# Kernel tuning notes

Hardware: AMD Instinct MI355X
Metric: run time of the kernel (lower is better)

## Reference

```python
import jax, jax.numpy as jnp
import numpy as np

B, S, D = 2, 2048, 1024   # batch, seq, hidden_size
H = 512                   # intermediate_size
E, K = 8, 2               # num_local_experts, num_experts_per_tok


def setup_inputs() -> dict:
    key = jax.random.key(0)
    k1, k2, k3, k4 = jax.random.split(key, 4)
    scale = 0.02
    return {
        "layer_input": jax.random.normal(k1, (B, S, D), dtype=jnp.float32),
        "w_router": jax.random.normal(k2, (E, D), dtype=jnp.float32) * scale,   # Linear(D, E, bias=False)
        "w_in": jax.random.normal(k3, (E, 2 * H, D), dtype=jnp.float32) * scale,  # ParallelExperts(E, D, 2H)
        "w_out": jax.random.normal(k4, (E, D, H), dtype=jnp.float32) * scale,     # ParallelExperts(E, H, D)
    }


def reference(layer_input, w_router, w_in, w_out):
    bsz, length, d = layer_input.shape
    x = layer_input.reshape(-1, d)                       # [T, D]
    T = x.shape[0]

    # ---- router (JetMoeTopKGating): top-k logits -> softmax gates ----
    router_logits = x @ w_router.T                       # [T, E], fp32
    top_v, top_i = jax.lax.top_k(router_logits, K)       # [T, K]
    top_gates = jax.nn.softmax(top_v, axis=-1)           # [T, K]
    # sparse gate matrix: zero except selected experts (equivalent to
    # torch's sort/gather/index_add dispatch-combine)
    gates = jnp.zeros((T, E), dtype=x.dtype).at[jnp.arange(T)[:, None], top_i].add(top_gates)  # [T, E]

    # ---- experts: fused SwiGLU FFN per expert; combine with sparse gates ----
    h = jnp.einsum('td,efd->tef', x, w_in)               # [T, E, 2H]
    a, b = jnp.split(h, 2, axis=-1)
    h = jax.nn.silu(a) * b                               # [T, E, H]
    y = jnp.einsum('teh,edh->ted', h, w_out)             # [T, E, D]
    out = jnp.einsum('te,ted->td', gates, y)             # [T, D]

    return out.reshape(bsz, length, d), router_logits
```

## Files before the change

### kernel.cpp

```cpp
#include <hip/hip_runtime.h>

typedef unsigned short u16;
typedef unsigned int   u32;

#define T_TOK 4096
#define D_DIM 1024
#define H_DIM 512
#define E_NUM 8
#define NP1   5120
#define MAXP  5120

typedef __bf16 bf16x8 __attribute__((ext_vector_type(8)));
typedef float  f32x4  __attribute__((ext_vector_type(4)));

__device__ __forceinline__ u16 f2bf(float f) {
    return __builtin_bit_cast(u16, (__bf16)f);
}
__device__ __forceinline__ u32 pk2(float a, float b) {
    return (u32)f2bf(a) | ((u32)f2bf(b) << 16);
}

__device__ __forceinline__ void gll16(const void* g, void* l) {
    __builtin_amdgcn_global_load_lds((const __attribute__((address_space(1))) void*)g,
                                     (__attribute__((address_space(3))) void*)l, 16, 0, 0);
}

#define LDFX(arr, r, ko) __builtin_bit_cast(bf16x8, \
    *(const uint4*)(&arr[r][((((ko) >> 3) ^ ((r) & 7)) << 3)]))
#define MFMA(a, b, c) __builtin_amdgcn_mfma_f32_16x16x32_bf16(a, b, c, 0, 0, 0)

__global__ __launch_bounds__(256) void fused_front(
    const float* __restrict__ x, const float* __restrict__ wr,
    const float* __restrict__ w_in, const float* __restrict__ w_out,
    float* __restrict__ logits_out, int* __restrict__ top_e, float* __restrict__ top_g,
    u16* __restrict__ xb, u16* __restrict__ wib, u16* __restrict__ wob,
    float* __restrict__ out_zero, int* __restrict__ e_init, int* __restrict__ blk_hist)
{
    const int bid = blockIdx.x;
    const int tid = threadIdx.x;

    if (bid >= 256) {
        const int b2 = bid - 256;
        if (b2 < 4096) {
            const size_t i = (size_t)b2 * 256 + tid;
            const float4 a = *(const float4*)(w_in + i * 8);
            const float4 b = *(const float4*)(w_in + i * 8 + 4);
            uint4 o;
            o.x = pk2(a.x, a.y); o.y = pk2(a.z, a.w);
            o.z = pk2(b.x, b.y); o.w = pk2(b.z, b.w);
            *(uint4*)(wib + i * 8) = o;
        } else if (b2 < 6144) {
            const size_t i = (size_t)(b2 - 4096) * 256 + tid;
            const float4 a = *(const float4*)(w_out + i * 8);
            const float4 b = *(const float4*)(w_out + i * 8 + 4);
            uint4 o;
            o.x = pk2(a.x, a.y); o.y = pk2(a.z, a.w);
            o.z = pk2(b.x, b.y); o.w = pk2(b.z, b.w);
            *(uint4*)(wob + i * 8) = o;
        } else if (b2 < 10240) {
            ((float4*)out_zero)[(size_t)(b2 - 6144) * 256 + tid] = make_float4(0.f, 0.f, 0.f, 0.f);
        } else {
            ((int4*)e_init)[(b2 - 10240) * 256 + tid] = make_int4(-1, -1, -1, -1);
        }
        return;
    }

    __shared__ float wrL[E_NUM][1024];
    __shared__ int   bh[16];
    if (tid < 16) bh[tid] = 0;
    #pragma unroll
    for (int i = 0; i < 8; ++i) {
        const int idx = (i * 256 + tid) * 4;
        *(float4*)&wrL[0][idx] = *(const float4*)(wr + idx);
    }
    __syncthreads();

    const int lane = tid & 63;
    const int wv   = tid >> 6;
    const int t0   = bid * 16 + wv * 4;

    for (int tt = 0; tt < 4; ++tt) {
        const int t = t0 + tt;
        const float* xr = x + ((size_t)t << 10);
        float4 xv[4];
        #pragma unroll
        for (int j = 0; j < 4; ++j)
            xv[j] = *(const float4*)(xr + j * 256 + lane * 4);

        #pragma unroll
        for (int j = 0; j < 4; ++j) {
            uint2 p;
            p.x = pk2(xv[j].x, xv[j].y);
            p.y = pk2(xv[j].z, xv[j].w);
            *(uint2*)(xb + ((size_t)t << 10) + j * 256 + lane * 4) = p;
        }

        float acc[E_NUM];
        #pragma unroll
        for (int e = 0; e < E_NUM; ++e) acc[e] = 0.f;
        #pragma unroll
        for (int j = 0; j < 4; ++j) {
            #pragma unroll
            for (int e = 0; e < E_NUM; ++e) {
                const float4 w4 = *(const float4*)&wrL[e][j * 256 + lane * 4];
                acc[e] += xv[j].x * w4.x + xv[j].y * w4.y + xv[j].z * w4.z + xv[j].w * w4.w;
            }
        }
        #pragma unroll
        for (int off = 32; off >= 1; off >>= 1) {
            #pragma unroll
            for (int e = 0; e < E_NUM; ++e)
                acc[e] += __shfl_xor(acc[e], off);
        }
        if (lane == 0) {
            #pragma unroll
            for (int e = 0; e < E_NUM; ++e)
                logits_out[t * E_NUM + e] = acc[e];
            int i0 = 0; float v0 = acc[0];
            #pragma unroll
            for (int e = 1; e < E_NUM; ++e) { if (acc[e] > v0) { v0 = acc[e]; i0 = e; } }
            int i1 = (i0 == 0) ? 1 : 0; float v1 = acc[i1];
            #pragma unroll
            for (int e = 0; e < E_NUM; ++e) { if (e != i0 && e != i1 && acc[e] > v1) { v1 = acc[e]; i1 = e; } }
            const float ed = __expf(v1 - v0);
            const float g0 = 1.f / (1.f + ed);
            top_e[2 * t]     = i0;  top_e[2 * t + 1] = i1;
            top_g[2 * t]     = g0;  top_g[2 * t + 1] = 1.f - g0;
            atomicAdd(&bh[2 * i0],     1);
            atomicAdd(&bh[2 * i1 + 1], 1);
        }
    }
    __syncthreads();
    if (tid < 16) blk_hist[bid * 16 + tid] = bh[tid];
}

__global__ __launch_bounds__(1024) void prep_kernel(
    const int* __restrict__ top_e, int* __restrict__ ws_i,
    int* __restrict__ e0, int* __restrict__ e1, const int* __restrict__ blk_hist)
{
    __shared__ int hist[16];
    __shared__ int cur[16];
    const int tid = threadIdx.x;
    if (tid < 16) hist[tid] = 0;
    __syncthreads();

    int part = 0;
    #pragma unroll
    for (int j = 0; j < 4; ++j) part += blk_hist[j * 1024 + tid];
    part += __shfl_xor(part, 16);
    part += __shfl_xor(part, 32);
    if ((tid & 63) < 16) atomicAdd(&hist[tid & 15], part);
    __syncthreads();

    if (tid == 0) {
        int off_[16];
        int s0 = 0, s1 = 0;
        for (int e = 0; e < E_NUM; ++e) {
            off_[2 * e]     = s0; s0 += (hist[2 * e]     + 127) & ~127;
            off_[2 * e + 1] = s1; s1 += (hist[2 * e + 1] + 127) & ~127;
        }
        int nt1 = 0;
        for (int e = 0; e < E_NUM; ++e) {
            for (int k = 0; k < 2; ++k) {
                const int b  = 2 * e + k;
                const int pc = (hist[b] + 127) & ~127;
                cur[b] = off_[b];
                for (int j = 0; j < pc / 128; ++j) {
                    const int rl = off_[b] + j * 128;
                    if (nt1 < 96) ws_i[512 + nt1++] = (e << 16) | (k * NP1 + rl);
                }
            }
        }
        ws_i[99] = nt1;
    }
    __syncthreads();

    const int4* t4 = (const int4*)top_e;
    const int4 a = t4[2 * tid];
    const int4 b = t4[2 * tid + 1];
    const int v[8] = {a.x, a.y, a.z, a.w, b.x, b.y, b.z, b.w};
    #pragma unroll
    for (int j = 0; j < 8; ++j) {
        const int i  = tid * 8 + j;
        const int bk = 2 * (v[j] & 7) + (j & 1);
        const int pos = atomicAdd(&cur[bk], 1);
        ((j & 1) ? e1 : e0)[pos] = i;
    }
}

__global__ __launch_bounds__(256, 2) void g1_a(
    const u16* __restrict__ xb, const u16* __restrict__ wib,
    const int* __restrict__ ws_i, const int* __restrict__ e0,
    const int* __restrict__ e1, u16* __restrict__ act)
{
    const int nt = ws_i[99];
    if ((int)blockIdx.y >= nt) return;
    const int tile = ws_i[512 + blockIdx.y];
    const int e  = tile >> 16;
    const int rb = tile & 0xFFFF;
    const int nc = blockIdx.x;

    __shared__ __align__(16) u16 xs[128][64];
    __shared__ __align__(16) u16 wt[128][64];
    __shared__ int tokL[128];

    const int tid = threadIdx.x;
    if (tid < 128) {
        const int ent = (rb >= NP1) ? e1[rb - NP1 + tid] : e0[rb + tid];
        tokL[tid] = (ent < 0) ? 0 : (ent >> 1);
    }
    __syncthreads();

    const int wid = tid >> 6, ln = tid & 63, qd = ln >> 4, lm = ln & 15;
    const int wrh = wid >> 1, wch = wid & 1;

    const u16* xsrc[4];
    const u16* wsrc[4];
    const u16* wbase = wib + ((size_t)e << 20);
    #pragma unroll
    for (int j = 0; j < 4; ++j) {
        const int r  = wid * 32 + j * 8 + (ln >> 3);
        const int sg = (ln & 7) ^ (r & 7);
        xsrc[j] = xb + ((size_t)tokL[r] << 10) + (sg << 3);
        const int h = r >> 6, r2 = r & 63;
        const int wrow = (r2 < 32) ? (nc * 64 + h * 32 + r2)
                                   : (512 + nc * 64 + h * 32 + (r2 - 32));
        wsrc[j] = wbase + ((size_t)wrow << 10) + (sg << 3);
    }

    f32x4 acc[4][4];
    #pragma unroll
    for (int i = 0; i < 4; ++i)
        #pragma unroll
        for (int j = 0; j < 4; ++j) acc[i][j] = (f32x4){0.f,0.f,0.f,0.f};

    for (int k0 = 0; k0 < 1024; k0 += 64) {
        #pragma unroll
        for (int j = 0; j < 4; ++j) {
            gll16(xsrc[j] + k0, &xs[wid * 32 + j * 8][0]);
            gll16(wsrc[j] + k0, &wt[wid * 32 + j * 8][0]);
        }
        __syncthreads();
        #pragma unroll
        for (int ki = 0; ki < 2; ++ki) {
            const int ko = ki * 32 + (qd << 3);
            bf16x8 aF[4], bF[4];
            #pragma unroll
            for (int i = 0; i < 4; ++i) aF[i] = LDFX(xs, wrh * 64 + i * 16 + lm, ko);
            #pragma unroll
            for (int j = 0; j < 4; ++j) bF[j] = LDFX(wt, wch * 64 + j * 16 + lm, ko);
            #pragma unroll
            for (int i = 0; i < 4; ++i)
                #pragma unroll
                for (int j = 0; j < 4; ++j)
                    acc[i][j] = MFMA(aF[i], bF[j], acc[i][j]);
        }
        __syncthreads();
    }

    #pragma unroll
    for (int i = 0; i < 4; ++i) {
        #pragma unroll
        for (int j = 0; j < 2; ++j) {
            #pragma unroll
            for (int r = 0; r < 4; ++r) {
                const float a = acc[i][j][r], b = acc[i][j + 2][r];
                const float v = b * a / (1.f + __expf(-a));
                const int row  = wrh * 64 + i * 16 + (qd << 2) + r;
                const int hcol = nc * 64 + wch * 32 + j * 16 + lm;
                act[((size_t)(rb + row) << 9) + hcol] = f2bf(v);
            }
        }
    }
}

__global__ __launch_bounds__(256, 2) void g2_a(
    const u16* __restrict__ act, const u16* __restrict__ wob,
    const int* __restrict__ ws_i, const int* __restrict__ e0,
    const int* __restrict__ e1, const float* __restrict__ top_g,
    float* __restrict__ out)
{
    const int nt = ws_i[99];
    if ((int)blockIdx.y >= nt) return;
    const int tile = ws_i[512 + blockIdx.y];
    const int e  = tile >> 16;
    const int rb = tile & 0xFFFF;
    const int dc = blockIdx.x;

    __shared__ __align__(16) u16 as_[128][64];
    __shared__ __align__(16) u16 wt2[128][64];
    __shared__ int   entL[128];
    __shared__ float gateL[128];

    const int tid = threadIdx.x;
    if (tid < 128) {
        const int ent = (rb >= NP1) ? e1[rb - NP1 + tid] : e0[rb + tid];
        entL[tid]  = ent;
        gateL[tid] = (ent < 0) ? 0.f : top_g[ent];
    }
    __syncthreads();

    const int wid = tid >> 6, ln = tid & 63, qd = ln >> 4, lm = ln & 15;
    const int wrh = wid >> 1, wch = wid & 1;

    const u16* asrc[4];
    const u16* wsrc[4];
    const u16* wbase = wob + ((size_t)e << 19);
    #pragma unroll
    for (int j = 0; j < 4; ++j) {
        const int r  = wid * 32 + j * 8 + (ln >> 3);
        const int sg = (ln & 7) ^ (r & 7);
        asrc[j] = act + ((size_t)(rb + r) << 9) + (sg << 3);
        wsrc[j] = wbase + ((size_t)((dc << 7) + r) << 9) + (sg << 3);
    }

    f32x4 acc[4][4];
    #pragma unroll
    for (int i = 0; i < 4; ++i)
        #pragma unroll
        for (int j = 0; j < 4; ++j) acc[i][j] = (f32x4){0.f,0.f,0.f,0.f};

    for (int k0 = 0; k0 < 512; k0 += 64) {
        #pragma unroll
        for (int j = 0; j < 4; ++j) {
            gll16(asrc[j] + k0, &as_[wid * 32 + j * 8][0]);
            gll16(wsrc[j] + k0, &wt2[wid * 32 + j * 8][0]);
        }
        __syncthreads();
        #pragma unroll
        for (int ki = 0; ki < 2; ++ki) {
            const int ko = ki * 32 + (qd << 3);
            bf16x8 aF[4], bF[4];
            #pragma unroll
            for (int i = 0; i < 4; ++i) aF[i] = LDFX(as_, wrh * 64 + i * 16 + lm, ko);
            #pragma unroll
            for (int j = 0; j < 4; ++j) bF[j] = LDFX(wt2, wch * 64 + j * 16 + lm, ko);
            #pragma unroll
            for (int i = 0; i < 4; ++i)
                #pragma unroll
                for (int j = 0; j < 4; ++j)
                    acc[i][j] = MFMA(aF[i], bF[j], acc[i][j]);
        }
        __syncthreads();
    }

    #pragma unroll
    for (int i = 0; i < 4; ++i) {
        #pragma unroll
        for (int j = 0; j < 4; ++j) {
            #pragma unroll
            for (int r = 0; r < 4; ++r) {
                const int row = wrh * 64 + i * 16 + (qd << 2) + r;
                const int ent = entL[row];
                if (ent >= 0) {
                    const int t   = ent >> 1;
                    const int col = (dc << 7) + wch * 64 + j * 16 + lm;
                    atomicAdd(out + ((size_t)t << 10) + col, gateL[row] * acc[i][j][r]);
                }
            }
        }
    }
}

extern "C" void kernel_launch(void* const* d_in, const int* in_sizes, int n_in,
                              void* d_out, int out_size, void* d_ws, size_t ws_size,
                              hipStream_t stream)
{
    (void)in_sizes; (void)n_in; (void)out_size; (void)ws_size;
    const float* x     = (const float*)d_in[0];
    const float* wr    = (const float*)d_in[1];
    const float* w_in  = (const float*)d_in[2];
    const float* w_out = (const float*)d_in[3];
    float* out = (float*)d_out;

    char* ws = (char*)d_ws;
    int*   ws_i     = (int*)ws;
    int*   e0       = (int*)(ws + 8192);
    int*   e1       = (int*)(ws + 28672);
    int*   top_e    = (int*)(ws + 49152);
    float* top_g    = (float*)(ws + 81920);
    int*   blk_hist = (int*)(ws + 114688);
    u16*   act      = (u16*)(ws + 147456);
    u16*   xb       = (u16*)(ws + 10633216);
    u16*   wib      = (u16*)(ws + 19021824);
    u16*   wob      = (u16*)(ws + 35799040);

    fused_front<<<10506, 256, 0, stream>>>(x, wr, w_in, w_out,
                                           out + (size_t)T_TOK * D_DIM,
                                           top_e, top_g, xb, wib, wob,
                                           out, e0, blk_hist);
    prep_kernel<<<1, 1024, 0, stream>>>(top_e, ws_i, e0, e1, blk_hist);
    g1_a<<<dim3(8, 80), 256, 0, stream>>>(xb, wib, ws_i, e0, e1, act);
    g2_a<<<dim3(8, 80), 256, 0, stream>>>(act, wob, ws_i, e0, e1, top_g, out);
}
```

Before: 183.6 us.

## Replace atomic scatter-add with per-slot bf16 buffer and combine kernel

The second expert GEMM now writes each gated (token, slot) result as bf16 into a scratch buffer indexed by the entry id, instead of doing fp32 atomicAdd into the output. A new combine kernel sums the two slots per token into the output. This also removes the output-zeroing blocks from the front kernel. The aim is to avoid atomic traffic and the zero-fill pass, at the cost of an extra kernel launch, an extra read/write pass, and bf16 rounding of partial results. The y buffer reuses the xb region, which is only safe because xb is dead by then.

```diff
diff --git a/kernel.cpp b/kernel.cpp
--- a/kernel.cpp
+++ b/kernel.cpp
@@ -19,6 +19,9 @@
 __device__ __forceinline__ u32 pk2(float a, float b) {
     return (u32)f2bf(a) | ((u32)f2bf(b) << 16);
 }
+__device__ __forceinline__ float bf2f(u32 lo16) {
+    return __builtin_bit_cast(float, lo16 << 16);
+}
 
 __device__ __forceinline__ void gll16(const void* g, void* l) {
     __builtin_amdgcn_global_load_lds((const __attribute__((address_space(1))) void*)g,
@@ -34,7 +37,7 @@
     const float* __restrict__ w_in, const float* __restrict__ w_out,
     float* __restrict__ logits_out, int* __restrict__ top_e, float* __restrict__ top_g,
     u16* __restrict__ xb, u16* __restrict__ wib, u16* __restrict__ wob,
-    float* __restrict__ out_zero, int* __restrict__ e_init, int* __restrict__ blk_hist)
+    int* __restrict__ e_init, int* __restrict__ blk_hist)
 {
     const int bid = blockIdx.x;
     const int tid = threadIdx.x;
@@ -57,10 +60,8 @@
             o.x = pk2(a.x, a.y); o.y = pk2(a.z, a.w);
             o.z = pk2(b.x, b.y); o.w = pk2(b.z, b.w);
             *(uint4*)(wob + i * 8) = o;
-        } else if (b2 < 10240) {
-            ((float4*)out_zero)[(size_t)(b2 - 6144) * 256 + tid] = make_float4(0.f, 0.f, 0.f, 0.f);
         } else {
-            ((int4*)e_init)[(b2 - 10240) * 256 + tid] = make_int4(-1, -1, -1, -1);
+            ((int4*)e_init)[(b2 - 6144) * 256 + tid] = make_int4(-1, -1, -1, -1);
         }
         return;
     }
@@ -278,7 +279,7 @@
     const u16* __restrict__ act, const u16* __restrict__ wob,
     const int* __restrict__ ws_i, const int* __restrict__ e0,
     const int* __restrict__ e1, const float* __restrict__ top_g,
-    float* __restrict__ out)
+    u16* __restrict__ y)
 {
     const int nt = ws_i[99];
     if ((int)blockIdx.y >= nt) return;
@@ -353,13 +354,34 @@
                 const int row = wrh * 64 + i * 16 + (qd << 2) + r;
                 const int ent = entL[row];
                 if (ent >= 0) {
-                    const int t   = ent >> 1;
                     const int col = (dc << 7) + wch * 64 + j * 16 + lm;
-                    atomicAdd(out + ((size_t)t << 10) + col, gateL[row] * acc[i][j][r]);
+                    y[((size_t)ent << 10) + col] = f2bf(gateL[row] * acc[i][j][r]);
                 }
             }
         }
     }
+}
+
+__global__ __launch_bounds__(256) void combine_kernel(
+    const u16* __restrict__ y, float* __restrict__ out)
+{
+    const int idx = blockIdx.x * 256 + threadIdx.x;
+    const int t = idx >> 7;
+    const int c = (idx & 127) << 3;
+    const uint4 a = *(const uint4*)(y + ((size_t)(2 * t)     << 10) + c);
+    const uint4 b = *(const uint4*)(y + ((size_t)(2 * t + 1) << 10) + c);
+    float4 o0, o1;
+    o0.x = bf2f(a.x & 0xFFFFu) + bf2f(b.x & 0xFFFFu);
+    o0.y = bf2f(a.x >> 16)     + bf2f(b.x >> 16);
+    o0.z = bf2f(a.y & 0xFFFFu) + bf2f(b.y & 0xFFFFu);
+    o0.w = bf2f(a.y >> 16)     + bf2f(b.y >> 16);
+    o1.x = bf2f(a.z & 0xFFFFu) + bf2f(b.z & 0xFFFFu);
+    o1.y = bf2f(a.z >> 16)     + bf2f(b.z >> 16);
+    o1.z = bf2f(a.w & 0xFFFFu) + bf2f(b.w & 0xFFFFu);
+    o1.w = bf2f(a.w >> 16)     + bf2f(b.w >> 16);
+    float* po = out + ((size_t)t << 10) + c;
+    *(float4*)po       = o0;
+    *(float4*)(po + 4) = o1;
 }
 
 extern "C" void kernel_launch(void* const* d_in, const int* in_sizes, int n_in,
@@ -383,13 +405,15 @@
     u16*   act      = (u16*)(ws + 147456);
     u16*   xb       = (u16*)(ws + 10633216);
     u16*   wib      = (u16*)(ws + 19021824);
+    u16*   y        = (u16*)(ws + 10633216);
     u16*   wob      = (u16*)(ws + 35799040);
 
-    fused_front<<<10506, 256, 0, stream>>>(x, wr, w_in, w_out,
-                                           out + (size_t)T_TOK * D_DIM,
-                                           top_e, top_g, xb, wib, wob,
-                                           out, e0, blk_hist);
+    fused_front<<<6410, 256, 0, stream>>>(x, wr, w_in, w_out,
+                                          out + (size_t)T_TOK * D_DIM,
+                                          top_e, top_g, xb, wib, wob,
+                                          e0, blk_hist);
     prep_kernel<<<1, 1024, 0, stream>>>(top_e, ws_i, e0, e1, blk_hist);
     g1_a<<<dim3(8, 80), 256, 0, stream>>>(xb, wib, ws_i, e0, e1, act);
-    g2_a<<<dim3(8, 80), 256, 0, stream>>>(act, wob, ws_i, e0, e1, top_g, out);
-}
+    g2_a<<<dim3(8, 80), 256, 0, stream>>>(act, wob, ws_i, e0, e1, top_g, y);
+    combine_kernel<<<2048, 256, 0, stream>>>(y, out);
+}
```

New measurement: 168.0 us. 1.09x faster.

## Split down-projection into two passes to replace atomics and drop output zeroing

Applied to the files above, without the earlier changes.

The down-projection GEMM is split into two launches, one for first-choice slots and one for second-choice slots. The first pass writes gated results directly and the second adds to them with a plain read-modify-write. This removes the float atomicAdds and the 16 MB output-zeroing pass in the front kernel. The GEMM grids are also flattened to 1D with a remapped tile index, so each group of eight consecutive blocks takes row tiles spread across experts, which may change cache locality. Correctness relies on every token appearing exactly once in each pass and on the second pass running only after the first finishes on the same stream.

```diff
diff --git a/kernel.cpp b/kernel.cpp
--- a/kernel.cpp
+++ b/kernel.cpp
@@ -34,7 +34,7 @@
     const float* __restrict__ w_in, const float* __restrict__ w_out,
     float* __restrict__ logits_out, int* __restrict__ top_e, float* __restrict__ top_g,
     u16* __restrict__ xb, u16* __restrict__ wib, u16* __restrict__ wob,
-    float* __restrict__ out_zero, int* __restrict__ e_init, int* __restrict__ blk_hist)
+    int* __restrict__ e_init, int* __restrict__ blk_hist)
 {
     const int bid = blockIdx.x;
     const int tid = threadIdx.x;
@@ -57,10 +57,8 @@
             o.x = pk2(a.x, a.y); o.y = pk2(a.z, a.w);
             o.z = pk2(b.x, b.y); o.w = pk2(b.z, b.w);
             *(uint4*)(wob + i * 8) = o;
-        } else if (b2 < 10240) {
-            ((float4*)out_zero)[(size_t)(b2 - 6144) * 256 + tid] = make_float4(0.f, 0.f, 0.f, 0.f);
         } else {
-            ((int4*)e_init)[(b2 - 10240) * 256 + tid] = make_int4(-1, -1, -1, -1);
+            ((int4*)e_init)[(b2 - 6144) * 256 + tid] = make_int4(-1, -1, -1, -1);
         }
         return;
     }
@@ -159,7 +157,7 @@
             off_[2 * e]     = s0; s0 += (hist[2 * e]     + 127) & ~127;
             off_[2 * e + 1] = s1; s1 += (hist[2 * e + 1] + 127) & ~127;
         }
-        int nt1 = 0;
+        int nt1 = 0, nt20 = 0, nt21 = 0;
         for (int e = 0; e < E_NUM; ++e) {
             for (int k = 0; k < 2; ++k) {
                 const int b  = 2 * e + k;
@@ -168,10 +166,14 @@
                 for (int j = 0; j < pc / 128; ++j) {
                     const int rl = off_[b] + j * 128;
                     if (nt1 < 96) ws_i[512 + nt1++] = (e << 16) | (k * NP1 + rl);
+                    if (k == 0) { if (nt20 < 48) ws_i[768 + nt20++] = (e << 16) | rl; }
+                    else        { if (nt21 < 48) ws_i[896 + nt21++] = (e << 16) | rl; }
                 }
             }
         }
-        ws_i[99] = nt1;
+        ws_i[99]  = nt1;
+        ws_i[100] = nt20;
+        ws_i[101] = nt21;
     }
     __syncthreads();
 
@@ -193,12 +195,14 @@
     const int* __restrict__ ws_i, const int* __restrict__ e0,
     const int* __restrict__ e1, u16* __restrict__ act)
 {
-    const int nt = ws_i[99];
-    if ((int)blockIdx.y >= nt) return;
-    const int tile = ws_i[512 + blockIdx.y];
+    const int nt  = ws_i[99];
+    const int bid = blockIdx.x;
+    const int ty  = (bid & 7) * 10 + ((bid >> 3) % 10);
+    const int nc  = bid / 80;
+    if (ty >= nt) return;
+    const int tile = ws_i[512 + ty];
     const int e  = tile >> 16;
     const int rb = tile & 0xFFFF;
-    const int nc = blockIdx.x;
 
     __shared__ __align__(16) u16 xs[128][64];
     __shared__ __align__(16) u16 wt[128][64];
@@ -276,16 +280,18 @@
 
 __global__ __launch_bounds__(256, 2) void g2_a(
     const u16* __restrict__ act, const u16* __restrict__ wob,
-    const int* __restrict__ ws_i, const int* __restrict__ e0,
-    const int* __restrict__ e1, const float* __restrict__ top_g,
-    float* __restrict__ out)
+    const int* __restrict__ ws_i, const int* __restrict__ entries,
+    const float* __restrict__ top_g, float* __restrict__ out, int pass)
 {
-    const int nt = ws_i[99];
-    if ((int)blockIdx.y >= nt) return;
-    const int tile = ws_i[512 + blockIdx.y];
-    const int e  = tile >> 16;
-    const int rb = tile & 0xFFFF;
-    const int dc = blockIdx.x;
+    const int nt  = ws_i[100 + pass];
+    const int bid = blockIdx.x;
+    const int ty  = (bid & 7) * 5 + ((bid >> 3) % 5);
+    const int dc  = bid / 40;
+    if (ty >= nt) return;
+    const int tile = ws_i[(pass ? 896 : 768) + ty];
+    const int e   = tile >> 16;
+    const int rbl = tile & 0xFFFF;
+    const int ab  = pass * NP1 + rbl;
 
     __shared__ __align__(16) u16 as_[128][64];
     __shared__ __align__(16) u16 wt2[128][64];
@@ -294,7 +300,7 @@
 
     const int tid = threadIdx.x;
     if (tid < 128) {
-        const int ent = (rb >= NP1) ? e1[rb - NP1 + tid] : e0[rb + tid];
+        const int ent = entries[rbl + tid];
         entL[tid]  = ent;
         gateL[tid] = (ent < 0) ? 0.f : top_g[ent];
     }
@@ -310,7 +316,7 @@
     for (int j = 0; j < 4; ++j) {
         const int r  = wid * 32 + j * 8 + (ln >> 3);
         const int sg = (ln & 7) ^ (r & 7);
-        asrc[j] = act + ((size_t)(rb + r) << 9) + (sg << 3);
+        asrc[j] = act + ((size_t)(ab + r) << 9) + (sg << 3);
         wsrc[j] = wbase + ((size_t)((dc << 7) + r) << 9) + (sg << 3);
     }
 
@@ -355,7 +361,10 @@
                 if (ent >= 0) {
                     const int t   = ent >> 1;
                     const int col = (dc << 7) + wch * 64 + j * 16 + lm;
-                    atomicAdd(out + ((size_t)t << 10) + col, gateL[row] * acc[i][j][r]);
+                    float* po = out + ((size_t)t << 10) + col;
+                    float v = gateL[row] * acc[i][j][r];
+                    if (pass) v += *po;
+                    *po = v;
                 }
             }
         }
@@ -385,11 +394,12 @@
     u16*   wib      = (u16*)(ws + 19021824);
     u16*   wob      = (u16*)(ws + 35799040);
 
-    fused_front<<<10506, 256, 0, stream>>>(x, wr, w_in, w_out,
-                                           out + (size_t)T_TOK * D_DIM,
-                                           top_e, top_g, xb, wib, wob,
-                                           out, e0, blk_hist);
+    fused_front<<<6410, 256, 0, stream>>>(x, wr, w_in, w_out,
+                                          out + (size_t)T_TOK * D_DIM,
+                                          top_e, top_g, xb, wib, wob,
+                                          e0, blk_hist);
     prep_kernel<<<1, 1024, 0, stream>>>(top_e, ws_i, e0, e1, blk_hist);
-    g1_a<<<dim3(8, 80), 256, 0, stream>>>(xb, wib, ws_i, e0, e1, act);
-    g2_a<<<dim3(8, 80), 256, 0, stream>>>(act, wob, ws_i, e0, e1, top_g, out);
-}
+    g1_a<<<640, 256, 0, stream>>>(xb, wib, ws_i, e0, e1, act);
+    g2_a<<<320, 256, 0, stream>>>(act, wob, ws_i, e0, top_g, out, 0);
+    g2_a<<<320, 256, 0, stream>>>(act, wob, ws_i, e1, top_g, out, 1);
+}
```

After: 186.9 us. About the same (+1.8%).
